# Kernel optimization log

Hardware: AMD Instinct MI355X
Metric: run time of the kernel (lower is better)

## Reference

```python
import jax, jax.numpy as jnp
import numpy as np
import math

V, B, C, H, W = 4, 8, 512, 16, 16
NH = 8


def setup_inputs() -> dict:
    key = jax.random.key(0)
    ks = jax.random.split(key, 10)
    def n(k, shape, s=1.0):
        return jax.random.normal(k, shape, dtype=jnp.float32) * s
    return dict(
        i=n(ks[0], (V, B, C, H, W)),
        c=n(ks[1], (V, B, C, H, W)),
        j=n(ks[2], (V, B, C, H, W)),
        ln1_g=jnp.ones((C,), jnp.float32), ln1_b=jnp.zeros((C,), jnp.float32),
        ln2_g=jnp.ones((C,), jnp.float32), ln2_b=jnp.zeros((C,), jnp.float32),
        Wq=n(ks[3], (C, C), 0.02), bq=jnp.zeros((C,), jnp.float32),
        Wkv=n(ks[4], (C, 2 * C), 0.02), bkv=jnp.zeros((2 * C,), jnp.float32),
        Wo=n(ks[5], (C, C), 0.02), bo=jnp.zeros((C,), jnp.float32),
        Wfc=n(ks[6], (C, 4 * C), 0.02), bfc=jnp.zeros((4 * C,), jnp.float32),
        Wpr=n(ks[7], (4 * C, C), 0.02), bpr=jnp.zeros((C,), jnp.float32),
    )


def _ln(x, g, b, eps=1e-5):
    mu = jnp.mean(x, axis=-1, keepdims=True)
    var = jnp.mean((x - mu) ** 2, axis=-1, keepdims=True)
    return (x - mu) * jax.lax.rsqrt(var + eps) * g + b


def _gelu_new(x):
    # 0.5*x*(1+tanh(sqrt(2/pi)*(x+0.044715*x^3)))
    k = math.sqrt(2.0 / math.pi)
    return 0.5 * x * (1.0 + jnp.tanh(k * (x + 0.044715 * x ** 3)))


def reference(i, c, j, ln1_g, ln1_b, ln2_g, ln2_b, Wq, bq, Wkv, bkv, Wo, bo, Wfc, bfc, Wpr, bpr):
    v, b, ch, h, w = i.shape
    T = v * h * w
    hd = ch // NH

    def to_seq(x):  # v b c h w -> b (v h w) c
        return jnp.transpose(x, (1, 0, 3, 4, 2)).reshape(b, T, ch)

    # LayerNorm (over channel dim) applied before attention
    qs = _ln(to_seq(i), ln1_g, ln1_b)   # [b, T, c]
    kvs = _ln(to_seq(j), ln1_g, ln1_b)  # [b, T, c]

    q = qs @ Wq + bq                    # [b, T, c]
    kv = kvs @ Wkv + bkv                # [b, T, 2c]
    k, vv = jnp.split(kv, 2, axis=-1)

    def heads(x):  # [b, T, c] -> [b, nh, T, hd]
        return x.reshape(b, T, NH, hd).transpose(0, 2, 1, 3)
    q, k, vv = heads(q), heads(k), heads(vv)

    # block-causal mask: token in view-block r attends to view-blocks <= r
    blk = jnp.arange(T) // (h * w)
    mask = blk[:, None] >= blk[None, :]  # [T, T] bool

    att = jnp.einsum('bhqd,bhkd->bhqk', q, k) * (1.0 / math.sqrt(hd))
    att = jnp.where(mask, att, -jnp.inf)
    att = jax.nn.softmax(att, axis=-1)
    y = jnp.einsum('bhqk,bhkd->bhqd', att, vv)
    y = y.transpose(0, 2, 1, 3).reshape(b, T, ch)
    y = y @ Wo + bo                     # attention output, seq layout

    # residual: ln1(c) + attn
    cs = _ln(to_seq(c), ln1_g, ln1_b) + y
    # MLP with residual
    hcs = _ln(cs, ln2_g, ln2_b)
    cs = cs + (_gelu_new(hcs @ Wfc + bfc) @ Wpr + bpr)

    # b (v h w) c -> v b c h w
    out = cs.reshape(b, v, h, w, ch).transpose(1, 0, 4, 2, 3)
    return out
```

## Files before the change

### kernel.cpp

```cpp
#include <hip/hip_runtime.h>
#include <hip/hip_bf16.h>
#include <math.h>


typedef __bf16 bf16;
typedef __bf16 bf16x8 __attribute__((ext_vector_type(8)));
typedef __bf16 bf16x4 __attribute__((ext_vector_type(4)));
typedef float  f32x4  __attribute__((ext_vector_type(4)));

__device__ __forceinline__ void gload_lds16(const void* g, void* l) {
  __builtin_amdgcn_global_load_lds(
      (__attribute__((address_space(1))) void*)(g),
      (__attribute__((address_space(3))) void*)(l), 16, 0, 0);
}

__global__ __launch_bounds__(256)
void prep_k(const float* __restrict__ Wq, const float* __restrict__ Wkv,
            const float* __restrict__ Wo, const float* __restrict__ Wfc,
            const float* __restrict__ Wpr,
            bf16* __restrict__ WqT, bf16* __restrict__ WkvT,
            bf16* __restrict__ WoT, bf16* __restrict__ WfcT,
            bf16* __restrict__ WprT,
            const float* __restrict__ xi, const float* __restrict__ xj,
            const float* __restrict__ xc,
            const float* __restrict__ g, const float* __restrict__ bb,
            bf16* __restrict__ qs, bf16* __restrict__ kvs,
            float* __restrict__ cs0)
{
  __shared__ float tt[32][33];
  __shared__ float red[4][32];
  const int t = blockIdx.x;
  const int tid = threadIdx.x;
  if (t < 3072) {
    const float* W; bf16* Wt; int K, N, lognx, tl;
    if (t < 256)       { W = Wq;  Wt = WqT;  K = 512;  N = 512;  lognx = 4; tl = t; }
    else if (t < 768)  { W = Wkv; Wt = WkvT; K = 512;  N = 1024; lognx = 5; tl = t - 256; }
    else if (t < 1024) { W = Wo;  Wt = WoT;  K = 512;  N = 512;  lognx = 4; tl = t - 768; }
    else if (t < 2048) { W = Wfc; Wt = WfcT; K = 512;  N = 2048; lognx = 6; tl = t - 1024; }
    else               { W = Wpr; Wt = WprT; K = 2048; N = 512;  lognx = 4; tl = t - 2048; }
    const int bx = tl & ((1 << lognx) - 1), by = tl >> lognx;
    const int x = tid & 31, y = tid >> 5;
    const int n0 = bx << 5, k0 = by << 5;
#pragma unroll
    for (int yy = y; yy < 32; yy += 8)
      tt[yy][x] = W[(size_t)(k0 + yy) * N + n0 + x];
    __syncthreads();
#pragma unroll
    for (int yy = y; yy < 32; yy += 8)
      Wt[(size_t)(n0 + yy) * K + k0 + x] = (bf16)tt[x][yy];
    return;
  }
  const int u = t - 3072;
  const int sel = u >> 9, bid = u & 511;
  const int hh = bid & 15, b = (bid >> 4) & 7, v = bid >> 7;
  const float* src = (sel == 0) ? xi : ((sel == 1) ? xj : xc);
  const size_t base = ((size_t)(v * 8 + b) * 512) * 256 + (size_t)hh * 16;
  const int q = tid & 3, chb = tid >> 2;
  const int wid = tid >> 6, lane = tid & 63;
  const int cb = chb << 3;

  float gr[8], br[8];
  *(f32x4*)&gr[0] = *(const f32x4*)&g[cb];
  *(f32x4*)&gr[4] = *(const f32x4*)&g[cb + 4];
  *(f32x4*)&br[0] = *(const f32x4*)&bb[cb];
  *(f32x4*)&br[4] = *(const f32x4*)&bb[cb + 4];

  f32x4 x[8];
#pragma unroll
  for (int k = 0; k < 8; ++k)
    x[k] = *(const f32x4*)&src[base + (size_t)(cb + k) * 256 + (q << 2)];

  float s[4] = {0.f, 0.f, 0.f, 0.f}, ss[4] = {0.f, 0.f, 0.f, 0.f};
#pragma unroll
  for (int k = 0; k < 8; ++k)
#pragma unroll
    for (int i = 0; i < 4; ++i) {
      s[i] += x[k][i];
      ss[i] += x[k][i] * x[k][i];
    }
#pragma unroll
  for (int off = 4; off < 64; off <<= 1)
#pragma unroll
    for (int i = 0; i < 4; ++i) {
      s[i] += __shfl_xor(s[i], off);
      ss[i] += __shfl_xor(ss[i], off);
    }
  if (lane < 16) {
    red[wid][(lane & 3) * 4 + (lane >> 2)]      = s[lane >> 2];
    red[wid][16 + (lane & 3) * 4 + (lane >> 2)] = ss[lane >> 2];
  }
  __syncthreads();
  float mu[4], rs[4];
#pragma unroll
  for (int i = 0; i < 4; ++i) {
    const int e = q * 4 + i;
    float st  = red[0][e] + red[1][e] + red[2][e] + red[3][e];
    float sst = red[0][16 + e] + red[1][16 + e] + red[2][16 + e] + red[3][16 + e];
    mu[i] = st * (1.f / 512.f);
    rs[i] = rsqrtf(sst * (1.f / 512.f) - mu[i] * mu[i] + 1e-5f);
  }
  const int tkb = v * 256 + hh * 16 + (q << 2);
  bf16* dstb = (sel == 0) ? qs : kvs;
#pragma unroll
  for (int i = 0; i < 4; ++i) {
    const size_t orow = ((size_t)b * 1024 + tkb + i) * 512;
    if (sel == 2) {
      f32x4 o0, o1;
#pragma unroll
      for (int k = 0; k < 4; ++k) {
        o0[k] = (x[k][i] - mu[i]) * rs[i] * gr[k] + br[k];
        o1[k] = (x[k + 4][i] - mu[i]) * rs[i] * gr[k + 4] + br[k + 4];
      }
      *(f32x4*)&cs0[orow + cb]     = o0;
      *(f32x4*)&cs0[orow + cb + 4] = o1;
    } else {
      bf16x8 o;
#pragma unroll
      for (int k = 0; k < 8; ++k)
        o[k] = (bf16)((x[k][i] - mu[i]) * rs[i] * gr[k] + br[k]);
      *(bf16x8*)&dstb[orow + cb] = o;
    }
  }
}

__global__ __launch_bounds__(256)
void ln2_k(const float* __restrict__ cs, const float* __restrict__ g,
           const float* __restrict__ bb, bf16* __restrict__ hcs)
{
  const int tid = threadIdx.x, wid = tid >> 6, lane = tid & 63;
  const int row = blockIdx.x * 4 + wid;
  const float* x = cs + (size_t)row * 512 + lane * 8;
  float v[8];
  *(f32x4*)&v[0] = *(const f32x4*)&x[0];
  *(f32x4*)&v[4] = *(const f32x4*)&x[4];
  float s = 0.f, ss = 0.f;
#pragma unroll
  for (int k = 0; k < 8; ++k) { s += v[k]; ss += v[k] * v[k]; }
#pragma unroll
  for (int off = 1; off < 64; off <<= 1) {
    s += __shfl_xor(s, off);
    ss += __shfl_xor(ss, off);
  }
  const float mu = s * (1.f / 512.f);
  const float rstd = rsqrtf(ss * (1.f / 512.f) - mu * mu + 1e-5f);
  bf16x8 o;
#pragma unroll
  for (int k = 0; k < 8; ++k) {
    int ch = lane * 8 + k;
    o[k] = (bf16)((v[k] - mu) * rstd * g[ch] + bb[ch]);
  }
  *(bf16x8*)&hcs[(size_t)row * 512 + lane * 8] = o;
}

__global__ __launch_bounds__(256)
void gemm_fc_k(const bf16* __restrict__ A, const bf16* __restrict__ Bt,
               const float* __restrict__ bias, bf16* __restrict__ fo)
{
  const int K = 512;
  __shared__ __align__(16) char smem[34816];
  bf16* As = (bf16*)smem;
  bf16* Bs = (bf16*)(smem + 16384);
  const int tid = threadIdx.x;
  const int wid = tid >> 6, lane = tid & 63;
  const int wr = wid >> 1, wc = wid & 1;
  const int ml = lane & 15, kg = (lane >> 4) << 3;
  const int m0 = blockIdx.x * 128, n0 = blockIdx.y * 128;

  const int e0 = wid * 512 + lane * 8;
  const int r0 = e0 >> 5, c0 = e0 & 31;
  const int e1 = e0 + 2048;
  const int r1 = e1 >> 5, c1 = e1 & 31;

  const bf16* Ag = A + (size_t)m0 * K;
  const bf16* Bg = Bt + (size_t)n0 * K;

  f32x4 acc[4][4] = {};

  gload_lds16(Ag + (size_t)r0 * K + c0, As + wid * 512);
  gload_lds16(Ag + (size_t)r1 * K + c1, As + 2048 + wid * 512);
  gload_lds16(Bg + (size_t)r0 * K + c0, Bs + wid * 512);
  gload_lds16(Bg + (size_t)r1 * K + c1, Bs + 2048 + wid * 512);

  int cur = 0;
  for (int k0 = 0; k0 < K; k0 += 32) {
    __syncthreads();
    if (k0 + 32 < K) {
      const int nb = cur ^ 1, kn = k0 + 32;
      gload_lds16(Ag + (size_t)r0 * K + kn + c0, As + nb * 4096 + wid * 512);
      gload_lds16(Ag + (size_t)r1 * K + kn + c1, As + nb * 4096 + 2048 + wid * 512);
      gload_lds16(Bg + (size_t)r0 * K + kn + c0, Bs + nb * 4096 + wid * 512);
      gload_lds16(Bg + (size_t)r1 * K + kn + c1, Bs + nb * 4096 + 2048 + wid * 512);
    }
    bf16x8 af[4], bfr[4];
#pragma unroll
    for (int mf = 0; mf < 4; ++mf)
      af[mf] = *(const bf16x8*)&As[cur * 4096 + (wr * 64 + mf * 16 + ml) * 32 + kg];
#pragma unroll
    for (int nf = 0; nf < 4; ++nf)
      bfr[nf] = *(const bf16x8*)&Bs[cur * 4096 + (wc * 64 + nf * 16 + ml) * 32 + kg];
#pragma unroll
    for (int mf = 0; mf < 4; ++mf)
#pragma unroll
      for (int nf = 0; nf < 4; ++nf)
        acc[mf][nf] = __builtin_amdgcn_mfma_f32_16x16x32_bf16(
            af[mf], bfr[nf], acc[mf][nf], 0, 0, 0);
    cur ^= 1;
  }

  __syncthreads();
  bf16* OT = (bf16*)smem;
  const int jrow0 = (lane >> 4) << 2;
#pragma unroll
  for (int nf = 0; nf < 4; ++nf) {
    const float bv = bias[n0 + wc * 64 + nf * 16 + ml];
#pragma unroll
    for (int mf = 0; mf < 4; ++mf)
#pragma unroll
      for (int j = 0; j < 4; ++j) {
        float x = acc[mf][nf][j] + bv;
        float u = 0.7978845608f * (x + 0.044715f * x * x * x);
        float e = __expf(2.f * u);
        float th = 1.f - 2.f / (e + 1.f);
        OT[(wr * 64 + mf * 16 + jrow0 + j) * 132 + wc * 64 + nf * 16 + ml] =
            (bf16)(0.5f * x * (1.f + th));
      }
  }
  __syncthreads();
#pragma unroll
  for (int it = 0; it < 8; ++it) {
    const int idx = it * 256 + tid;
    const int cg = idx & 15, r = idx >> 4;
    *(bf16x8*)&fo[(size_t)(m0 + r) * 2048 + n0 + cg * 8] =
        *(const bf16x8*)&OT[r * 132 + cg * 8];
  }
}

enum { EPI_O = 2, EPI_PR = 4 };

template <int EPI>
__global__ __launch_bounds__(512)
void gemmsk_k(const bf16* __restrict__ A, const bf16* __restrict__ Bt,
              const float* __restrict__ bias, const float* res,
              void* out0, int K)
{
  __shared__ __align__(16) char smem[65536];
  bf16*  AS = (bf16*)smem;
  bf16*  BS = (bf16*)(smem + 32768);
  float* CF = (float*)smem;

  const int tid = threadIdx.x;
  const int wid = tid >> 6, lane = tid & 63;
  const int half = wid >> 2, w2 = wid & 3;
  const int wr = w2 >> 1, wc = w2 & 1;
  const int ml = lane & 15, kg = (lane >> 4) << 3;
  const int m0 = blockIdx.x * 128, n0 = blockIdx.y * 128;
  const int Kh = K >> 1;

  const int e0 = w2 * 512 + lane * 8;
  const int r0 = e0 >> 5, c0 = e0 & 31;
  const int e1 = e0 + 2048;
  const int r1 = e1 >> 5, c1 = e1 & 31;

  const bf16* Ag = A + (size_t)m0 * K + half * Kh;
  const bf16* Bg = Bt + (size_t)n0 * K + half * Kh;
  bf16* A0 = AS + half * 4096;
  bf16* B0 = BS + half * 4096;

  f32x4 acc[4][4] = {};

  gload_lds16(Ag + (size_t)r0 * K + c0, A0 + w2 * 512);
  gload_lds16(Ag + (size_t)r1 * K + c1, A0 + 2048 + w2 * 512);
  gload_lds16(Bg + (size_t)r0 * K + c0, B0 + w2 * 512);
  gload_lds16(Bg + (size_t)r1 * K + c1, B0 + 2048 + w2 * 512);

  int cur = 0;
  for (int k0 = 0; k0 < Kh; k0 += 32) {
    __syncthreads();
    if (k0 + 32 < Kh) {
      const int kn = k0 + 32;
      bf16* An = AS + ((cur ^ 1) * 8192) + half * 4096;
      bf16* Bn = BS + ((cur ^ 1) * 8192) + half * 4096;
      gload_lds16(Ag + (size_t)r0 * K + kn + c0, An + w2 * 512);
      gload_lds16(Ag + (size_t)r1 * K + kn + c1, An + 2048 + w2 * 512);
      gload_lds16(Bg + (size_t)r0 * K + kn + c0, Bn + w2 * 512);
      gload_lds16(Bg + (size_t)r1 * K + kn + c1, Bn + 2048 + w2 * 512);
    }
    const bf16* Ac = AS + cur * 8192 + half * 4096;
    const bf16* Bc = BS + cur * 8192 + half * 4096;
    bf16x8 af[4], bfr[4];
#pragma unroll
    for (int mf = 0; mf < 4; ++mf)
      af[mf] = *(const bf16x8*)&Ac[(wr * 64 + mf * 16 + ml) * 32 + kg];
#pragma unroll
    for (int nf = 0; nf < 4; ++nf)
      bfr[nf] = *(const bf16x8*)&Bc[(wc * 64 + nf * 16 + ml) * 32 + kg];
#pragma unroll
    for (int mf = 0; mf < 4; ++mf)
#pragma unroll
      for (int nf = 0; nf < 4; ++nf)
        acc[mf][nf] = __builtin_amdgcn_mfma_f32_16x16x32_bf16(
            af[mf], bfr[nf], acc[mf][nf], 0, 0, 0);
    cur ^= 1;
  }

  const int jrow0 = (lane >> 4) << 2;
  __syncthreads();
  if (half == 0) {
#pragma unroll
    for (int mf = 0; mf < 4; ++mf)
#pragma unroll
      for (int nf = 0; nf < 4; ++nf)
#pragma unroll
        for (int j = 0; j < 4; ++j)
          CF[(wr * 64 + mf * 16 + jrow0 + j) * 128 + wc * 64 + nf * 16 + ml] =
              acc[mf][nf][j];
  }
  __syncthreads();
  if (half == 1) {
#pragma unroll
    for (int nf = 0; nf < 4; ++nf) {
      const int n = n0 + wc * 64 + nf * 16 + ml;
      const float bv = bias[n];
#pragma unroll
      for (int mf = 0; mf < 4; ++mf) {
        const int mbase = m0 + wr * 64 + mf * 16 + jrow0;
        float v4[4];
#pragma unroll
        for (int j = 0; j < 4; ++j)
          v4[j] = acc[mf][nf][j] +
                  CF[(wr * 64 + mf * 16 + jrow0 + j) * 128 + wc * 64 + nf * 16 + ml];
        if constexpr (EPI == EPI_O) {
          float* cs = (float*)out0;
#pragma unroll
          for (int j = 0; j < 4; ++j) {
            const size_t idx = (size_t)(mbase + j) * 512 + n;
            cs[idx] = v4[j] + bv + res[idx];
          }
        } else {
          float* out = (float*)out0;
          const int b = mbase >> 10, t = mbase & 1023;
          const int v = t >> 8, hhh = (t >> 4) & 15, w0 = t & 15;
          f32x4 o;
#pragma unroll
          for (int j = 0; j < 4; ++j)
            o[j] = v4[j] + bv + res[(size_t)(mbase + j) * 512 + n];
          *(f32x4*)&out[(((size_t)v * 8 + b) * 512 + n) * 256 + hhh * 16 + w0] = o;
        }
      }
    }
  }
}

__global__ __launch_bounds__(256)
void gemm_qkv_k(const bf16* __restrict__ Aq, const bf16* __restrict__ Akv,
                const bf16* __restrict__ WqT, const bf16* __restrict__ WkvT,
                const float* __restrict__ bq, const float* __restrict__ bkv,
                bf16* __restrict__ q_buf, bf16* __restrict__ k_buf,
                bf16* __restrict__ v_t)
{
  const int K = 512;
  __shared__ __align__(16) char smem[34816];
  bf16* As = (bf16*)smem;
  bf16* Bs = (bf16*)(smem + 16384);
  const int tid = threadIdx.x;
  const int wid = tid >> 6, lane = tid & 63;
  const int wr = wid >> 1, wc = wid & 1;
  const int ml = lane & 15, kg = (lane >> 4) << 3;
  const int ybl = blockIdx.y;
  const bool isq = ybl < 4;
  const bf16* A     = isq ? Aq  : Akv;
  const bf16* Bt    = isq ? WqT : WkvT;
  const float* bias = isq ? bq : bkv;
  const int n0 = isq ? (ybl << 7) : ((ybl - 4) << 7);
  const int m0 = blockIdx.x * 128;

  const int e0 = wid * 512 + lane * 8;
  const int r0 = e0 >> 5, c0 = e0 & 31;
  const int e1 = e0 + 2048;
  const int r1 = e1 >> 5, c1 = e1 & 31;

  const bf16* Ag = A + (size_t)m0 * K;
  const bf16* Bg = Bt + (size_t)n0 * K;

  f32x4 acc[4][4] = {};

  gload_lds16(Ag + (size_t)r0 * K + c0, As + wid * 512);
  gload_lds16(Ag + (size_t)r1 * K + c1, As + 2048 + wid * 512);
  gload_lds16(Bg + (size_t)r0 * K + c0, Bs + wid * 512);
  gload_lds16(Bg + (size_t)r1 * K + c1, Bs + 2048 + wid * 512);

  int cur = 0;
  for (int k0 = 0; k0 < K; k0 += 32) {
    __syncthreads();
    if (k0 + 32 < K) {
      const int nb = cur ^ 1, kn = k0 + 32;
      gload_lds16(Ag + (size_t)r0 * K + kn + c0, As + nb * 4096 + wid * 512);
      gload_lds16(Ag + (size_t)r1 * K + kn + c1, As + nb * 4096 + 2048 + wid * 512);
      gload_lds16(Bg + (size_t)r0 * K + kn + c0, Bs + nb * 4096 + wid * 512);
      gload_lds16(Bg + (size_t)r1 * K + kn + c1, Bs + nb * 4096 + 2048 + wid * 512);
    }
    bf16x8 af[4], bfr[4];
#pragma unroll
    for (int mf = 0; mf < 4; ++mf)
      af[mf] = *(const bf16x8*)&As[cur * 4096 + (wr * 64 + mf * 16 + ml) * 32 + kg];
#pragma unroll
    for (int nf = 0; nf < 4; ++nf)
      bfr[nf] = *(const bf16x8*)&Bs[cur * 4096 + (wc * 64 + nf * 16 + ml) * 32 + kg];
#pragma unroll
    for (int mf = 0; mf < 4; ++mf)
#pragma unroll
      for (int nf = 0; nf < 4; ++nf)
        acc[mf][nf] = __builtin_amdgcn_mfma_f32_16x16x32_bf16(
            af[mf], bfr[nf], acc[mf][nf], 0, 0, 0);
    cur ^= 1;
  }

  __syncthreads();
  bf16* OT = (bf16*)smem;
  const int jrow0 = (lane >> 4) << 2;
  const int b = m0 >> 10, t0 = m0 & 1023;
  if (ybl < 8) {
#pragma unroll
    for (int nf = 0; nf < 4; ++nf) {
      const float bv = bias[n0 + wc * 64 + nf * 16 + ml];
#pragma unroll
      for (int mf = 0; mf < 4; ++mf)
#pragma unroll
        for (int j = 0; j < 4; ++j)
          OT[(wr * 64 + mf * 16 + jrow0 + j) * 132 + wc * 64 + nf * 16 + ml] =
              (bf16)(acc[mf][nf][j] + bv);
    }
    __syncthreads();
    bf16* dst = isq ? q_buf : k_buf;
    const int h0 = n0 >> 6;
#pragma unroll
    for (int it = 0; it < 8; ++it) {
      const int idx = it * 256 + tid;
      const int dg = idx & 7, r = (idx >> 3) & 127, hl = idx >> 10;
      *(bf16x8*)&dst[(((size_t)b * 8 + h0 + hl) * 1024 + t0 + r) * 64 + dg * 8] =
          *(const bf16x8*)&OT[r * 132 + hl * 64 + dg * 8];
    }
  } else {
#pragma unroll
    for (int nf = 0; nf < 4; ++nf) {
      const float bv = bias[n0 + wc * 64 + nf * 16 + ml];
#pragma unroll
      for (int mf = 0; mf < 4; ++mf) {
        bf16x4 o;
#pragma unroll
        for (int j = 0; j < 4; ++j) o[j] = (bf16)(acc[mf][nf][j] + bv);
        *(bf16x4*)&OT[(wc * 64 + nf * 16 + ml) * 132 + wr * 64 + mf * 16 + jrow0] = o;
      }
    }
    __syncthreads();
    const int h0 = (n0 - 512) >> 6;
#pragma unroll
    for (int it = 0; it < 8; ++it) {
      const int idx = it * 256 + tid;
      const int og = idx & 15, c = idx >> 4;
      const int hl = c >> 6, d = c & 63;
      *(bf16x8*)&v_t[(((size_t)b * 8 + h0 + hl) * 64 + d) * 1024 + t0 + og * 8] =
          *(const bf16x8*)&OT[c * 132 + og * 8];
    }
  }
}

__global__ __launch_bounds__(256)
void attn_k(const bf16* __restrict__ qb, const bf16* __restrict__ kb,
            const bf16* __restrict__ vt, bf16* __restrict__ y)
{
  __shared__ bf16 Ks[2][4096];
  __shared__ bf16 Vs[2][4096];
  __shared__ bf16 Ps[4][1024];
  const int tid = threadIdx.x, wid = tid >> 6, lane = tid & 63;
  const int L = blockIdx.x;
  const int xcd = L & 7, chunk = L >> 3;
  const int bh = xcd + ((chunk >> 4) << 3);
  const int qt = 15 - (chunk & 15);
  const int b = bh >> 3, h = bh & 7;
  const int t0 = qt << 6;
  const int ml = lane & 15, hi = lane >> 4, kg = hi << 3;

  const bf16* qrow = qb + ((size_t)bh * 1024 + t0 + wid * 16) * 64;
  bf16x8 aq[2];
  aq[0] = *(const bf16x8*)&qrow[ml * 64 + kg];
  aq[1] = *(const bf16x8*)&qrow[ml * 64 + 32 + kg];

  f32x4 accO[4] = {};
  float lsum[4] = {0.f, 0.f, 0.f, 0.f};

  const int nkt = ((qt >> 2) + 1) << 2;
  const bf16* kbase = kb + (size_t)bh * 1024 * 64;
  const bf16* vbase = vt + (size_t)bh * 64 * 1024;

  const int sr = (wid << 3) + (lane >> 3);
  const int sg = ((lane & 7) ^ ((lane >> 3) & 7)) << 3;
  bf16* pw = &Ps[wid][0];

  {
    gload_lds16(kbase + (size_t)sr * 64 + sg,          &Ks[0][wid * 512]);
    gload_lds16(kbase + (size_t)(sr + 32) * 64 + sg,   &Ks[0][2048 + wid * 512]);
    gload_lds16(vbase + (size_t)sr * 1024 + sg,        &Vs[0][wid * 512]);
    gload_lds16(vbase + (size_t)(sr + 32) * 1024 + sg, &Vs[0][2048 + wid * 512]);
  }

  int cur = 0;
  for (int kt = 0; kt < nkt; ++kt) {
    __syncthreads();
    if (kt + 1 < nkt) {
      const int tk0 = (kt + 1) << 6;
      const int nb = cur ^ 1;
      gload_lds16(kbase + (size_t)(tk0 + sr) * 64 + sg,        &Ks[nb][wid * 512]);
      gload_lds16(kbase + (size_t)(tk0 + sr + 32) * 64 + sg,   &Ks[nb][2048 + wid * 512]);
      gload_lds16(vbase + (size_t)sr * 1024 + tk0 + sg,        &Vs[nb][wid * 512]);
      gload_lds16(vbase + (size_t)(sr + 32) * 1024 + tk0 + sg, &Vs[nb][2048 + wid * 512]);
    }

    f32x4 sa[4] = {};
#pragma unroll
    for (int nf = 0; nf < 4; ++nf) {
      const int row = nf * 16 + ml;
#pragma unroll
      for (int ks = 0; ks < 2; ++ks) {
        const int g = ((ks * 4 + hi) ^ (ml & 7)) << 3;
        bf16x8 bk = *(const bf16x8*)&Ks[cur][row * 64 + g];
        sa[nf] = __builtin_amdgcn_mfma_f32_16x16x32_bf16(aq[ks], bk, sa[nf], 0, 0, 0);
      }
    }

#pragma unroll
    for (int nf = 0; nf < 4; ++nf) {
      const int gp0 = nf * 2 + (ml >> 3);
#pragma unroll
      for (int j = 0; j < 4; ++j) {
        const float p = __expf(sa[nf][j] * 0.125f);
        lsum[j] += p;
        const int prow = (hi << 2) + j;
        pw[prow * 64 + ((gp0 ^ (prow & 7)) << 3) + (ml & 7)] = (bf16)p;
      }
    }

#pragma unroll
    for (int ks = 0; ks < 2; ++ks) {
      const int g = ((ks * 4 + hi) ^ (ml & 7)) << 3;
      bf16x8 pa = *(const bf16x8*)&pw[ml * 64 + g];
#pragma unroll
      for (int df = 0; df < 4; ++df) {
        bf16x8 bv = *(const bf16x8*)&Vs[cur][(df * 16 + ml) * 64 + g];
        accO[df] = __builtin_amdgcn_mfma_f32_16x16x32_bf16(pa, bv, accO[df], 0, 0, 0);
      }
    }
    cur ^= 1;
  }

  float inv[4];
#pragma unroll
  for (int j = 0; j < 4; ++j) {
    float s = lsum[j];
#pragma unroll
    for (int off = 1; off < 16; off <<= 1) s += __shfl_xor(s, off);
    inv[j] = 1.f / s;
  }
#pragma unroll
  for (int df = 0; df < 4; ++df)
#pragma unroll
    for (int j = 0; j < 4; ++j) {
      const int t = t0 + wid * 16 + (hi << 2) + j;
      const int c = h * 64 + df * 16 + ml;
      y[((size_t)b * 1024 + t) * 512 + c] = (bf16)(accO[df][j] * inv[j]);
    }
}

extern "C" void kernel_launch(void* const* d_in, const int* in_sizes, int n_in,
                              void* d_out, int out_size, void* d_ws, size_t ws_size,
                              hipStream_t stream)
{
  const float* xi    = (const float*)d_in[0];
  const float* xc    = (const float*)d_in[1];
  const float* xj    = (const float*)d_in[2];
  const float* ln1_g = (const float*)d_in[3];
  const float* ln1_b = (const float*)d_in[4];
  const float* ln2_g = (const float*)d_in[5];
  const float* ln2_b = (const float*)d_in[6];
  const float* Wq    = (const float*)d_in[7];
  const float* bq    = (const float*)d_in[8];
  const float* Wkv   = (const float*)d_in[9];
  const float* bkv   = (const float*)d_in[10];
  const float* Wo    = (const float*)d_in[11];
  const float* bo    = (const float*)d_in[12];
  const float* Wfc   = (const float*)d_in[13];
  const float* bfc   = (const float*)d_in[14];
  const float* Wpr   = (const float*)d_in[15];
  const float* bpr   = (const float*)d_in[16];

  char* ws = (char*)d_ws;
  const size_t MB = 1ull << 20;
  bf16*  qs    = (bf16*)(ws + 0);
  bf16*  kvs   = (bf16*)(ws + 8 * MB);
  float* cs0   = (float*)(ws + 16 * MB);
  bf16*  WqT   = (bf16*)(ws + 32 * MB);
  bf16*  WkvT  = (bf16*)(ws + 32 * MB + 512 * 1024);
  bf16*  WoT   = (bf16*)(ws + 33 * MB + 512 * 1024);
  bf16*  WfcT  = (bf16*)(ws + 34 * MB);
  bf16*  WprT  = (bf16*)(ws + 36 * MB);
  bf16*  q_buf = (bf16*)(ws + 38 * MB);
  bf16*  k_buf = (bf16*)(ws + 46 * MB);
  bf16*  v_t   = (bf16*)(ws + 54 * MB);
  bf16*  yb    = (bf16*)(ws + 0);
  bf16*  hcs   = (bf16*)(ws + 8 * MB);
  bf16*  fcact = (bf16*)(ws + 38 * MB);
  float* cs    = cs0;

  prep_k<<<dim3(4608), 256, 0, stream>>>(Wq, Wkv, Wo, Wfc, Wpr,
                                         WqT, WkvT, WoT, WfcT, WprT,
                                         xi, xj, xc, ln1_g, ln1_b, qs, kvs, cs0);

  gemm_qkv_k<<<dim3(64, 12), 256, 0, stream>>>(qs, kvs, WqT, WkvT, bq, bkv,
                                               q_buf, k_buf, v_t);

  attn_k<<<dim3(1024), 256, 0, stream>>>(q_buf, k_buf, v_t, yb);

  gemmsk_k<EPI_O><<<dim3(64, 4), 512, 0, stream>>>(yb, WoT, bo, cs0,
                                                   (void*)cs, 512);

  ln2_k<<<dim3(2048), 256, 0, stream>>>(cs, ln2_g, ln2_b, hcs);

  gemm_fc_k<<<dim3(64, 16), 256, 0, stream>>>(hcs, WfcT, bfc, fcact);

  gemmsk_k<EPI_PR><<<dim3(64, 4), 512, 0, stream>>>(fcact, WprT, bpr, cs,
                                                    d_out, 2048);

  (void)in_sizes; (void)n_in; (void)out_size; (void)ws_size;
}
```

Measured before the change: 182.7 us.

## Store residual stream in bf16, halve split-K GEMM M tile, add MFMA priority hints

The residual stream (ln1(c) and the post-attention sum) is now stored in bf16 instead of fp32, which halves traffic in prep, the Wo epilogue, ln2 and the final projection epilogue. The split-K GEMM tile shrinks from 128 to 64 rows, doubling the grid to 512 blocks for better CU fill and cutting LDS use. s_setprio hints are placed around the MFMA sections of the attention kernel to favour matrix issue. Storing the residual in bf16 lowers output precision.

Result: faster. 169.9 us (-7.0%).

```diff
diff --git a/kernel.cpp b/kernel.cpp
--- a/kernel.cpp
+++ b/kernel.cpp
@@ -25,7 +25,7 @@
             const float* __restrict__ xc,
             const float* __restrict__ g, const float* __restrict__ bb,
             bf16* __restrict__ qs, bf16* __restrict__ kvs,
-            float* __restrict__ cs0)
+            bf16* __restrict__ csb)
 {
   __shared__ float tt[32][33];
   __shared__ float red[4][32];
@@ -100,39 +100,28 @@
     rs[i] = rsqrtf(sst * (1.f / 512.f) - mu[i] * mu[i] + 1e-5f);
   }
   const int tkb = v * 256 + hh * 16 + (q << 2);
-  bf16* dstb = (sel == 0) ? qs : kvs;
+  bf16* dstb = (sel == 0) ? qs : ((sel == 1) ? kvs : csb);
 #pragma unroll
   for (int i = 0; i < 4; ++i) {
     const size_t orow = ((size_t)b * 1024 + tkb + i) * 512;
-    if (sel == 2) {
-      f32x4 o0, o1;
-#pragma unroll
-      for (int k = 0; k < 4; ++k) {
-        o0[k] = (x[k][i] - mu[i]) * rs[i] * gr[k] + br[k];
-        o1[k] = (x[k + 4][i] - mu[i]) * rs[i] * gr[k + 4] + br[k + 4];
-      }
-      *(f32x4*)&cs0[orow + cb]     = o0;
-      *(f32x4*)&cs0[orow + cb + 4] = o1;
-    } else {
-      bf16x8 o;
-#pragma unroll
-      for (int k = 0; k < 8; ++k)
-        o[k] = (bf16)((x[k][i] - mu[i]) * rs[i] * gr[k] + br[k]);
-      *(bf16x8*)&dstb[orow + cb] = o;
-    }
+    bf16x8 o;
+#pragma unroll
+    for (int k = 0; k < 8; ++k)
+      o[k] = (bf16)((x[k][i] - mu[i]) * rs[i] * gr[k] + br[k]);
+    *(bf16x8*)&dstb[orow + cb] = o;
   }
 }
 
 __global__ __launch_bounds__(256)
-void ln2_k(const float* __restrict__ cs, const float* __restrict__ g,
+void ln2_k(const bf16* __restrict__ cs, const float* __restrict__ g,
            const float* __restrict__ bb, bf16* __restrict__ hcs)
 {
   const int tid = threadIdx.x, wid = tid >> 6, lane = tid & 63;
   const int row = blockIdx.x * 4 + wid;
-  const float* x = cs + (size_t)row * 512 + lane * 8;
+  const bf16x8 v8 = *(const bf16x8*)&cs[(size_t)row * 512 + lane * 8];
   float v[8];
-  *(f32x4*)&v[0] = *(const f32x4*)&x[0];
-  *(f32x4*)&v[4] = *(const f32x4*)&x[4];
+#pragma unroll
+  for (int k = 0; k < 8; ++k) v[k] = (float)v8[k];
   float s = 0.f, ss = 0.f;
 #pragma unroll
   for (int k = 0; k < 8; ++k) { s += v[k]; ss += v[k] * v[k]; }
@@ -240,12 +229,12 @@
 template <int EPI>
 __global__ __launch_bounds__(512)
 void gemmsk_k(const bf16* __restrict__ A, const bf16* __restrict__ Bt,
-              const float* __restrict__ bias, const float* res,
+              const float* __restrict__ bias, const bf16* res,
               void* out0, int K)
 {
-  __shared__ __align__(16) char smem[65536];
+  __shared__ __align__(16) char smem[49152];
   bf16*  AS = (bf16*)smem;
-  bf16*  BS = (bf16*)(smem + 32768);
+  bf16*  BS = (bf16*)(smem + 16384);
   float* CF = (float*)smem;
 
   const int tid = threadIdx.x;
@@ -253,49 +242,48 @@
   const int half = wid >> 2, w2 = wid & 3;
   const int wr = w2 >> 1, wc = w2 & 1;
   const int ml = lane & 15, kg = (lane >> 4) << 3;
-  const int m0 = blockIdx.x * 128, n0 = blockIdx.y * 128;
+  const int m0 = blockIdx.x * 64, n0 = blockIdx.y * 128;
   const int Kh = K >> 1;
 
-  const int e0 = w2 * 512 + lane * 8;
-  const int r0 = e0 >> 5, c0 = e0 & 31;
-  const int e1 = e0 + 2048;
-  const int r1 = e1 >> 5, c1 = e1 & 31;
+  const int eA = w2 * 512 + lane * 8;
+  const int rA = eA >> 5, cA = eA & 31;
+  const int eB0 = (w2 * 2) * 512 + lane * 8;
+  const int rB0 = eB0 >> 5, cB0 = eB0 & 31;
+  const int eB1 = eB0 + 512;
+  const int rB1 = eB1 >> 5, cB1 = eB1 & 31;
 
   const bf16* Ag = A + (size_t)m0 * K + half * Kh;
   const bf16* Bg = Bt + (size_t)n0 * K + half * Kh;
-  bf16* A0 = AS + half * 4096;
-  bf16* B0 = BS + half * 4096;
-
-  f32x4 acc[4][4] = {};
-
-  gload_lds16(Ag + (size_t)r0 * K + c0, A0 + w2 * 512);
-  gload_lds16(Ag + (size_t)r1 * K + c1, A0 + 2048 + w2 * 512);
-  gload_lds16(Bg + (size_t)r0 * K + c0, B0 + w2 * 512);
-  gload_lds16(Bg + (size_t)r1 * K + c1, B0 + 2048 + w2 * 512);
+
+  f32x4 acc[2][4] = {};
+
+  gload_lds16(Ag + (size_t)rA * K + cA, AS + half * 2048 + w2 * 512);
+  gload_lds16(Bg + (size_t)rB0 * K + cB0, BS + half * 4096 + (w2 * 2) * 512);
+  gload_lds16(Bg + (size_t)rB1 * K + cB1, BS + half * 4096 + (w2 * 2 + 1) * 512);
 
   int cur = 0;
   for (int k0 = 0; k0 < Kh; k0 += 32) {
     __syncthreads();
     if (k0 + 32 < Kh) {
-      const int kn = k0 + 32;
-      bf16* An = AS + ((cur ^ 1) * 8192) + half * 4096;
-      bf16* Bn = BS + ((cur ^ 1) * 8192) + half * 4096;
-      gload_lds16(Ag + (size_t)r0 * K + kn + c0, An + w2 * 512);
-      gload_lds16(Ag + (size_t)r1 * K + kn + c1, An + 2048 + w2 * 512);
-      gload_lds16(Bg + (size_t)r0 * K + kn + c0, Bn + w2 * 512);
-      gload_lds16(Bg + (size_t)r1 * K + kn + c1, Bn + 2048 + w2 * 512);
-    }
-    const bf16* Ac = AS + cur * 8192 + half * 4096;
+      const int kn = k0 + 32, nb = cur ^ 1;
+      gload_lds16(Ag + (size_t)rA * K + kn + cA,
+                  AS + nb * 4096 + half * 2048 + w2 * 512);
+      gload_lds16(Bg + (size_t)rB0 * K + kn + cB0,
+                  BS + nb * 8192 + half * 4096 + (w2 * 2) * 512);
+      gload_lds16(Bg + (size_t)rB1 * K + kn + cB1,
+                  BS + nb * 8192 + half * 4096 + (w2 * 2 + 1) * 512);
+    }
+    const bf16* Ac = AS + cur * 4096 + half * 2048;
     const bf16* Bc = BS + cur * 8192 + half * 4096;
-    bf16x8 af[4], bfr[4];
-#pragma unroll
-    for (int mf = 0; mf < 4; ++mf)
-      af[mf] = *(const bf16x8*)&Ac[(wr * 64 + mf * 16 + ml) * 32 + kg];
+    bf16x8 af[2], bfr[4];
+#pragma unroll
+    for (int mf = 0; mf < 2; ++mf)
+      af[mf] = *(const bf16x8*)&Ac[(wr * 32 + mf * 16 + ml) * 32 + kg];
 #pragma unroll
     for (int nf = 0; nf < 4; ++nf)
       bfr[nf] = *(const bf16x8*)&Bc[(wc * 64 + nf * 16 + ml) * 32 + kg];
 #pragma unroll
-    for (int mf = 0; mf < 4; ++mf)
+    for (int mf = 0; mf < 2; ++mf)
 #pragma unroll
       for (int nf = 0; nf < 4; ++nf)
         acc[mf][nf] = __builtin_amdgcn_mfma_f32_16x16x32_bf16(
@@ -307,12 +295,12 @@
   __syncthreads();
   if (half == 0) {
 #pragma unroll
-    for (int mf = 0; mf < 4; ++mf)
+    for (int mf = 0; mf < 2; ++mf)
 #pragma unroll
       for (int nf = 0; nf < 4; ++nf)
 #pragma unroll
         for (int j = 0; j < 4; ++j)
-          CF[(wr * 64 + mf * 16 + jrow0 + j) * 128 + wc * 64 + nf * 16 + ml] =
+          CF[(wr * 32 + mf * 16 + jrow0 + j) * 128 + wc * 64 + nf * 16 + ml] =
               acc[mf][nf][j];
   }
   __syncthreads();
@@ -322,19 +310,19 @@
       const int n = n0 + wc * 64 + nf * 16 + ml;
       const float bv = bias[n];
 #pragma unroll
-      for (int mf = 0; mf < 4; ++mf) {
-        const int mbase = m0 + wr * 64 + mf * 16 + jrow0;
+      for (int mf = 0; mf < 2; ++mf) {
+        const int mbase = m0 + wr * 32 + mf * 16 + jrow0;
         float v4[4];
 #pragma unroll
         for (int j = 0; j < 4; ++j)
           v4[j] = acc[mf][nf][j] +
-                  CF[(wr * 64 + mf * 16 + jrow0 + j) * 128 + wc * 64 + nf * 16 + ml];
+                  CF[(wr * 32 + mf * 16 + jrow0 + j) * 128 + wc * 64 + nf * 16 + ml];
         if constexpr (EPI == EPI_O) {
-          float* cs = (float*)out0;
+          bf16* cs = (bf16*)out0;
 #pragma unroll
           for (int j = 0; j < 4; ++j) {
             const size_t idx = (size_t)(mbase + j) * 512 + n;
-            cs[idx] = v4[j] + bv + res[idx];
+            cs[idx] = (bf16)(v4[j] + bv + (float)res[idx]);
           }
         } else {
           float* out = (float*)out0;
@@ -343,7 +331,7 @@
           f32x4 o;
 #pragma unroll
           for (int j = 0; j < 4; ++j)
-            o[j] = v4[j] + bv + res[(size_t)(mbase + j) * 512 + n];
+            o[j] = v4[j] + bv + (float)res[(size_t)(mbase + j) * 512 + n];
           *(f32x4*)&out[(((size_t)v * 8 + b) * 512 + n) * 256 + hhh * 16 + w0] = o;
         }
       }
@@ -517,6 +505,7 @@
     }
 
     f32x4 sa[4] = {};
+    __builtin_amdgcn_s_setprio(1);
 #pragma unroll
     for (int nf = 0; nf < 4; ++nf) {
       const int row = nf * 16 + ml;
@@ -527,6 +516,7 @@
         sa[nf] = __builtin_amdgcn_mfma_f32_16x16x32_bf16(aq[ks], bk, sa[nf], 0, 0, 0);
       }
     }
+    __builtin_amdgcn_s_setprio(0);
 
 #pragma unroll
     for (int nf = 0; nf < 4; ++nf) {
@@ -540,6 +530,7 @@
       }
     }
 
+    __builtin_amdgcn_s_setprio(1);
 #pragma unroll
     for (int ks = 0; ks < 2; ++ks) {
       const int g = ((ks * 4 + hi) ^ (ml & 7)) << 3;
@@ -550,6 +541,7 @@
         accO[df] = __builtin_amdgcn_mfma_f32_16x16x32_bf16(pa, bv, accO[df], 0, 0, 0);
       }
     }
+    __builtin_amdgcn_s_setprio(0);
     cur ^= 1;
   }
 
@@ -597,7 +589,7 @@
   const size_t MB = 1ull << 20;
   bf16*  qs    = (bf16*)(ws + 0);
   bf16*  kvs   = (bf16*)(ws + 8 * MB);
-  float* cs0   = (float*)(ws + 16 * MB);
+  bf16*  csb   = (bf16*)(ws + 16 * MB);
   bf16*  WqT   = (bf16*)(ws + 32 * MB);
   bf16*  WkvT  = (bf16*)(ws + 32 * MB + 512 * 1024);
   bf16*  WoT   = (bf16*)(ws + 33 * MB + 512 * 1024);
@@ -609,26 +601,25 @@
   bf16*  yb    = (bf16*)(ws + 0);
   bf16*  hcs   = (bf16*)(ws + 8 * MB);
   bf16*  fcact = (bf16*)(ws + 38 * MB);
-  float* cs    = cs0;
 
   prep_k<<<dim3(4608), 256, 0, stream>>>(Wq, Wkv, Wo, Wfc, Wpr,
                                          WqT, WkvT, WoT, WfcT, WprT,
-                                         xi, xj, xc, ln1_g, ln1_b, qs, kvs, cs0);
+                                         xi, xj, xc, ln1_g, ln1_b, qs, kvs, csb);
 
   gemm_qkv_k<<<dim3(64, 12), 256, 0, stream>>>(qs, kvs, WqT, WkvT, bq, bkv,
                                                q_buf, k_buf, v_t);
 
   attn_k<<<dim3(1024), 256, 0, stream>>>(q_buf, k_buf, v_t, yb);
 
-  gemmsk_k<EPI_O><<<dim3(64, 4), 512, 0, stream>>>(yb, WoT, bo, cs0,
-                                                   (void*)cs, 512);
-
-  ln2_k<<<dim3(2048), 256, 0, stream>>>(cs, ln2_g, ln2_b, hcs);
+  gemmsk_k<EPI_O><<<dim3(128, 4), 512, 0, stream>>>(yb, WoT, bo, csb,
+                                                    (void*)csb, 512);
+
+  ln2_k<<<dim3(2048), 256, 0, stream>>>(csb, ln2_g, ln2_b, hcs);
 
   gemm_fc_k<<<dim3(64, 16), 256, 0, stream>>>(hcs, WfcT, bfc, fcact);
 
-  gemmsk_k<EPI_PR><<<dim3(64, 4), 512, 0, stream>>>(fcact, WprT, bpr, cs,
-                                                    d_out, 2048);
+  gemmsk_k<EPI_PR><<<dim3(128, 4), 512, 0, stream>>>(fcact, WprT, bpr, csb,
+                                                     d_out, 2048);
 
   (void)in_sizes; (void)n_in; (void)out_size; (void)ws_size;
 }
```
